# Kernel tuning notes

Measured on AMD Instinct MI355X. Metric: run time of the kernel, lower is better.

The kernel has to match this reference:

```python
import jax, jax.numpy as jnp
import numpy as np

B = 32; H = 56; W = 56; C = 384; NH = 12; WS = 14; SS = 7
L = H * W; N = WS * WS; HD = C // NH; SCALE = HD ** -0.5; HID = 4 * C
NW = (H // WS) * (W // WS)
EPS = 1e-5

def _relative_index():
    ch = np.arange(WS)[:, None].repeat(WS, 1)
    cw = np.arange(WS)[None, :].repeat(WS, 0)
    coords = np.stack([ch, cw], -1).reshape(-1, 2)  # [N,2]
    rel = coords[:, None, :] - coords[None, :, :]
    rel = rel + (WS - 1)
    rel[:, :, 0] *= 2 * WS - 1
    return rel.sum(-1)  # [N,N], values in [0,(2WS-1)^2)

def _attn_mask():
    img = np.zeros((H, W))
    sl = (slice(0, -WS), slice(-WS, -SS), slice(-SS, None))
    cnt = 0
    for hs in sl:
        for ws_ in sl:
            img[hs, ws_] = cnt; cnt += 1
    mw = img.reshape(H // WS, WS, W // WS, WS).transpose(0, 2, 1, 3).reshape(-1, N)
    am = mw[:, None, :] - mw[:, :, None]  # [nW,N,N]
    return np.where(am != 0, -100.0, 0.0).astype(np.float32)

REL_IDX = jnp.asarray(_relative_index())
MASK = jnp.asarray(_attn_mask())  # [NW,N,N]

def _ln(x, w, b):
    m = jnp.mean(x, -1, keepdims=True)
    v = jnp.mean((x - m) ** 2, -1, keepdims=True)
    return (x - m) * jax.lax.rsqrt(v + EPS) * w + b

def setup_inputs() -> dict:
    key = jax.random.key(0)
    ks = jax.random.split(key, 8)
    s = 0.02
    return {
        "x": jax.random.normal(ks[0], (B, L, C), jnp.float32),
        "norm1_w": jnp.ones((C,), jnp.float32),
        "norm1_b": jnp.zeros((C,), jnp.float32),
        "qkv_w": jax.random.normal(ks[1], (3 * C, C), jnp.float32) * s,
        "qkv_b": jnp.zeros((3 * C,), jnp.float32),
        "proj_w": jax.random.normal(ks[2], (C, C), jnp.float32) * s,
        "proj_b": jnp.zeros((C,), jnp.float32),
        "relative_table": jax.random.normal(ks[3], ((2 * WS - 1) ** 2, 2 * NH), jnp.float32) * s,
        "norm2_w": jnp.ones((C,), jnp.float32),
        "norm2_b": jnp.zeros((C,), jnp.float32),
        "fc1_w": jax.random.normal(ks[4], (HID, C), jnp.float32) * s,
        "fc1_b": jnp.zeros((HID,), jnp.float32),
        "fc2_w": jax.random.normal(ks[5], (C, HID), jnp.float32) * s,
        "fc2_b": jnp.zeros((C,), jnp.float32),
    }

def reference(x, norm1_w, norm1_b, qkv_w, qkv_b, proj_w, proj_b,
              relative_table, norm2_w, norm2_b, fc1_w, fc1_b, fc2_w, fc2_b):
    shortcut = x
    xn = _ln(x, norm1_w, norm1_b).reshape(B, H, W, C)
    # cyclic shift + window partition -> [B*NW, N, C]
    xs = jnp.roll(xn, (-SS, -SS), (1, 2))
    xw = xs.reshape(B, H // WS, WS, W // WS, WS, C).transpose(0, 1, 3, 2, 4, 5).reshape(-1, N, C)
    B_ = B * NW
    qkv = (xw @ qkv_w.T + qkv_b).reshape(B_, N, 3, NH, HD).transpose(2, 0, 3, 1, 4)
    q, k, v = qkv[0] * SCALE, qkv[1], qkv[2]  # [B_,NH,N,HD]
    attn = jnp.einsum('bhnd,bhmd->bhnm', q, k)  # [B_,NH,N,N]
    rel = relative_table[REL_IDX]  # [N,N,2*NH]
    rel = rel.transpose(2, 0, 1)  # [2*NH,N,N]
    bias, rscale = rel[:NH], rel[NH:]
    attn = attn + bias[None]
    attn = attn.reshape(B, NW, NH, N, N) + MASK[None, :, None]
    attn = jax.nn.softmax(attn.reshape(B_, NH, N, N), axis=-1)
    attn = attn * rscale[None]  # multiplicative relative scale AFTER softmax
    out = jnp.einsum('bhnm,bhmd->bhnd', attn, v)
    out = out.transpose(0, 2, 1, 3).reshape(B_, N, C)
    out = out @ proj_w.T + proj_b
    # window reverse + reverse shift
    xr = out.reshape(B, H // WS, W // WS, WS, WS, C).transpose(0, 1, 3, 2, 4, 5).reshape(B, H, W, C)
    xr = jnp.roll(xr, (SS, SS), (1, 2)).reshape(B, L, C)
    x = shortcut + xr
    h = _ln(x, norm2_w, norm2_b)
    h = jax.nn.gelu(h @ fc1_w.T + fc1_b, approximate=False) @ fc2_w.T + fc2_b
    return x + h
```

## Files before the change

kernel.cpp:

```cpp
#include <hip/hip_runtime.h>
#include <hip/hip_bf16.h>
#include <math.h>

#define BDIM 32
#define HDIM 56
#define WDIM 56
#define CDIM 384
#define NHEAD 12
#define WSZ 14
#define SSZ 7
#define LDIM (HDIM*WDIM)
#define NTOK (WSZ*WSZ)
#define HDHEAD (CDIM/NHEAD)
#define HIDDIM (4*CDIM)
#define NWIN 16
#define BWIN (BDIM*NWIN)
#define MROWS (BDIM*LDIM)
#define EPSLN 1e-5f
#define ATTSCALE 0.17677669529663687f

typedef __hip_bfloat16 bf16;
typedef __attribute__((ext_vector_type(8))) short bf16x8;
typedef __attribute__((ext_vector_type(4))) float f32x4;

#define ASYNC16(gp, lp) __builtin_amdgcn_global_load_lds( \
    (__attribute__((address_space(1))) void*)(gp),        \
    (__attribute__((address_space(3))) void*)(lp), 16, 0, 0)

static __device__ __forceinline__ short f2bfs(float x) {
  union { bf16 h; short s; } u; u.h = __float2bfloat16(x); return u.s;
}

__global__ __launch_bounds__(256) void k_cvt(const float* __restrict__ in,
                                             bf16* __restrict__ out, int n)
{
  int i = blockIdx.x * 256 + threadIdx.x;
  if (i < n) out[i] = __float2bfloat16(in[i]);
}

template<bool WIN>
__global__ __launch_bounds__(128) void k_ln(const float* __restrict__ xin,
    const float* __restrict__ gw, const float* __restrict__ gb,
    bf16* __restrict__ out)
{
  int r = blockIdx.x;
  int t = threadIdx.x;
  const float* xp = xin + (size_t)r * CDIM;
  float v0 = xp[t], v1 = xp[t+128], v2 = xp[t+256];
  float s  = v0+v1+v2;
  float ss = v0*v0 + v1*v1 + v2*v2;
  #pragma unroll
  for (int o = 32; o > 0; o >>= 1) { s += __shfl_down(s, o); ss += __shfl_down(ss, o); }
  __shared__ float red[4];
  if ((t & 63) == 0) { red[(t>>6)*2] = s; red[(t>>6)*2+1] = ss; }
  __syncthreads();
  float mean = (red[0]+red[2]) * (1.0f/CDIM);
  float var  = (red[1]+red[3]) * (1.0f/CDIM) - mean*mean;
  float rstd = rsqrtf(var + EPSLN);

  size_t orow;
  if (WIN) {
    int b = r / LDIM, l = r % LDIM;
    int h = l / WDIM, w = l % WDIM;
    int h2 = (h + HDIM - SSZ) % HDIM, w2 = (w + WDIM - SSZ) % WDIM;
    int wh = h2 / WSZ, ii = h2 % WSZ, ww = w2 / WSZ, jj = w2 % WSZ;
    int b_ = b*NWIN + wh*4 + ww;
    int n  = ii*WSZ + jj;
    orow = ((size_t)b_*NTOK + n) * CDIM;
  } else {
    orow = (size_t)r * CDIM;
  }
  out[orow+t]     = __float2bfloat16((v0-mean)*rstd*gw[t]     + gb[t]);
  out[orow+t+128] = __float2bfloat16((v1-mean)*rstd*gw[t+128] + gb[t+128]);
  out[orow+t+256] = __float2bfloat16((v2-mean)*rstd*gw[t+256] + gb[t+256]);
}

template<int KD, int EPI>
__global__ __launch_bounds__(256) void k_mgemm(
    const bf16* __restrict__ A, const bf16* __restrict__ Wb,
    const float* __restrict__ bias, const float* __restrict__ aux,
    float* __restrict__ outf, bf16* __restrict__ outb)
{
  __shared__ short As[128*32];
  __shared__ short Bs[128*32];
  int tid  = threadIdx.x;
  int lane = tid & 63, wid = tid >> 6;
  int wr = wid >> 1, wc = wid & 1;
  int row0 = blockIdx.y * 128, col0 = blockIdx.x * 128;

  f32x4 acc[4][4] = {};

  int srow[2];
  int skk = (lane & 3) * 8;
  #pragma unroll
  for (int s = 0; s < 2; s++) {
    int c = wid*2 + s;
    srow[s] = c*16 + (lane >> 2);
  }

  for (int k0 = 0; k0 < KD; k0 += 32) {
    #pragma unroll
    for (int s = 0; s < 2; s++) {
      int c = wid*2 + s;
      ASYNC16(A  + (size_t)(row0 + srow[s])*KD + k0 + skk, &As[c*512]);
      ASYNC16(Wb + (size_t)(col0 + srow[s])*KD + k0 + skk, &Bs[c*512]);
    }
    __syncthreads();

    bf16x8 af[4], bfr[4];
    #pragma unroll
    for (int m = 0; m < 4; m++)
      af[m] = *reinterpret_cast<const bf16x8*>(
          &As[(wr*64 + m*16 + (lane & 15))*32 + ((lane >> 4) * 8)]);
    #pragma unroll
    for (int n = 0; n < 4; n++)
      bfr[n] = *reinterpret_cast<const bf16x8*>(
          &Bs[(wc*64 + n*16 + (lane & 15))*32 + ((lane >> 4) * 8)]);
    #pragma unroll
    for (int m = 0; m < 4; m++)
      #pragma unroll
      for (int n = 0; n < 4; n++)
        acc[m][n] = __builtin_amdgcn_mfma_f32_16x16x32_bf16(af[m], bfr[n], acc[m][n], 0, 0, 0);
    __syncthreads();
  }

  int crow = row0 + wr*64 + ((lane >> 4) * 4);
  int ccol = col0 + wc*64 + (lane & 15);
  #pragma unroll
  for (int m = 0; m < 4; m++) {
    #pragma unroll
    for (int i = 0; i < 4; i++) {
      int r = crow + m*16 + i;
      if constexpr (EPI == 0) {
        int b_ = r / NTOK, nn = r % NTOK;
        const size_t QKVSTRIDE = (size_t)BWIN*NHEAD*NTOK*HDHEAD;
        #pragma unroll
        for (int n = 0; n < 4; n++) {
          int c = ccol + n*16;
          float val = acc[m][n][i] + bias[c];
          int which = c / CDIM, rem = c - which*CDIM;
          int hh = rem >> 5, dd = rem & 31;
          if (which == 0) val *= ATTSCALE;
          outb[(size_t)which*QKVSTRIDE + (((size_t)b_*NHEAD+hh)*NTOK+nn)*HDHEAD + dd]
              = __float2bfloat16(val);
        }
      } else if constexpr (EPI == 1) {
        int b_ = r / NTOK, nn = r % NTOK;
        int b = b_ >> 4, wi = b_ & 15, wh = wi >> 2, ww = wi & 3;
        int ii = nn / WSZ, jj = nn % WSZ;
        int hh = (wh*WSZ + ii + SSZ) % HDIM;
        int wcc = (ww*WSZ + jj + SSZ) % WDIM;
        size_t rr = ((size_t)b*LDIM + hh*WDIM + wcc) * CDIM;
        #pragma unroll
        for (int n = 0; n < 4; n++) {
          int c = ccol + n*16;
          outf[rr+c] = aux[rr+c] + acc[m][n][i] + bias[c];
        }
      } else if constexpr (EPI == 2) {
        #pragma unroll
        for (int n = 0; n < 4; n++) {
          int c = ccol + n*16;
          float val = acc[m][n][i] + bias[c];
          val = 0.5f * val * (1.0f + erff(val * 0.70710678118654752f));
          outb[(size_t)r*HIDDIM + c] = __float2bfloat16(val);
        }
      } else {
        #pragma unroll
        for (int n = 0; n < 4; n++) {
          int c = ccol + n*16;
          outf[(size_t)r*CDIM + c] = acc[m][n][i] + bias[c] + aux[(size_t)r*CDIM + c];
        }
      }
    }
  }
}

__global__ __launch_bounds__(256) void k_attn_mfma(const bf16* __restrict__ q,
    const bf16* __restrict__ k, const bf16* __restrict__ v,
    const float* __restrict__ rt, bf16* __restrict__ out)
{
  __shared__ short  Ks[208*32];
  __shared__ short  Vt[32*224];
  __shared__ short  Ps[4][16*224];
  __shared__ float2 tab2[729];
  __shared__ int    regv[208];

  int blk = blockIdx.x;
  int b_ = blk / NHEAD, head = blk % NHEAD;
  int tid = threadIdx.x, lane = tid & 63, wid = tid >> 6;
  int c15 = lane & 15, h4 = lane >> 4;

  const bf16* kp = k + (size_t)blk*NTOK*HDHEAD;
  const bf16* vp = v + (size_t)blk*NTOK*HDHEAD;
  for (int c = tid; c < 784; c += 256) {
    int m = c >> 2, k8 = (c & 3) * 8;
    *(bf16x8*)&Ks[m*32 + k8] = *(const bf16x8*)(kp + m*32 + k8);
    bf16x8 vv = *(const bf16x8*)(vp + m*32 + k8);
    #pragma unroll
    for (int j = 0; j < 8; j++) Vt[(k8+j)*224 + m] = vv[j];
  }
  for (int e = tid; e < 12*32; e += 256) Ks[196*32 + e] = 0;
  for (int e = tid; e < 32*28; e += 256) Vt[(e/28)*224 + 196 + (e%28)] = 0;
  for (int e = tid; e < 729; e += 256)
    tab2[e] = make_float2(rt[e*2*NHEAD + head], rt[e*2*NHEAD + NHEAD + head]);
  {
    int wi = b_ & 15, wh = wi >> 2, ww = wi & 3;
    for (int e = tid; e < 208; e += 256) {
      int rv = 0;
      if (e < NTOK) {
        int i = e / WSZ, j = e % WSZ;
        int ha = wh*WSZ + i, wa = ww*WSZ + j;
        int rh = ha < (HDIM-WSZ) ? 0 : (ha < (HDIM-SSZ) ? 1 : 2);
        int rw = wa < (WDIM-WSZ) ? 0 : (wa < (WDIM-SSZ) ? 1 : 2);
        rv = rh*3 + rw;
      }
      regv[e] = rv;
    }
  }
  __syncthreads();

  int   moff[13], mreg[13];
  float mpad[13];
  #pragma unroll
  for (int t = 0; t < 13; t++) {
    int m  = t*16 + c15;
    int mm = min(m, NTOK-1);
    moff[t] = (mm/WSZ)*27 + (mm%WSZ);
    mreg[t] = regv[mm];
    mpad[t] = (m >= NTOK) ? -1e30f : 0.f;
  }

  short* myP = &Ps[wid][0];
  #pragma unroll
  for (int i = 0; i < 4; i++) myP[(h4*4+i)*224 + 208 + c15] = 0;

  bf16* op = out + (size_t)b_*NTOK*CDIM + head*HDHEAD;

  for (int t4 = 0; t4 < 4; t4++) {
    int s = t4*4 + wid;
    int qrow = min(s*16 + c15, NTOK-1);
    bf16x8 qf = *(const bf16x8*)(q + ((size_t)blk*NTOK + qrow)*HDHEAD + h4*8);

    f32x4 sc[13];
    #pragma unroll
    for (int t = 0; t < 13; t++) {
      bf16x8 kf = *(const bf16x8*)&Ks[(t*16 + c15)*32 + h4*8];
      sc[t] = __builtin_amdgcn_mfma_f32_16x16x32_bf16(qf, kf, (f32x4){0.f,0.f,0.f,0.f}, 0, 0, 0);
    }

    #pragma unroll
    for (int i = 0; i < 4; i++) {
      int n  = s*16 + h4*4 + i;
      int nc = min(n, NTOK-1);
      int nbase = ((nc/WSZ) + 13)*27 + (nc%WSZ) + 13;
      int nreg  = regv[nc];
      float rr[13];
      float mx = -1e30f;
      #pragma unroll
      for (int t = 0; t < 13; t++) {
        float2 hr = tab2[nbase - moff[t]];
        float sv = sc[t][i] + hr.x + ((mreg[t] != nreg) ? -100.f : 0.f) + mpad[t];
        rr[t] = hr.y;
        sc[t][i] = sv;
        mx = fmaxf(mx, sv);
      }
      #pragma unroll
      for (int o = 1; o < 16; o <<= 1) mx = fmaxf(mx, __shfl_xor(mx, o));
      float sum = 0.f;
      #pragma unroll
      for (int t = 0; t < 13; t++) {
        float e = __expf(sc[t][i] - mx);
        sc[t][i] = e; sum += e;
      }
      #pragma unroll
      for (int o = 1; o < 16; o <<= 1) sum += __shfl_xor(sum, o);
      float inv = 1.f / sum;
      int prow = h4*4 + i;
      #pragma unroll
      for (int t = 0; t < 13; t++)
        myP[prow*224 + t*16 + c15] = f2bfs(sc[t][i] * inv * rr[t]);
    }

    __syncthreads();

    f32x4 o0 = {0.f,0.f,0.f,0.f}, o1 = {0.f,0.f,0.f,0.f};
    #pragma unroll
    for (int t7 = 0; t7 < 7; t7++) {
      bf16x8 pf = *(const bf16x8*)&myP[c15*224 + t7*32 + h4*8];
      bf16x8 v0 = *(const bf16x8*)&Vt[c15*224 + t7*32 + h4*8];
      bf16x8 v1 = *(const bf16x8*)&Vt[(16 + c15)*224 + t7*32 + h4*8];
      o0 = __builtin_amdgcn_mfma_f32_16x16x32_bf16(pf, v0, o0, 0, 0, 0);
      o1 = __builtin_amdgcn_mfma_f32_16x16x32_bf16(pf, v1, o1, 0, 0, 0);
    }

    #pragma unroll
    for (int i = 0; i < 4; i++) {
      int n = s*16 + h4*4 + i;
      if (n < NTOK) {
        op[(size_t)n*CDIM + c15]      = __float2bfloat16(o0[i]);
        op[(size_t)n*CDIM + 16 + c15] = __float2bfloat16(o1[i]);
      }
    }

    __syncthreads();
  }
}

extern "C" void kernel_launch(void* const* d_in, const int* in_sizes, int n_in,
                              void* d_out, int out_size, void* d_ws, size_t ws_size,
                              hipStream_t stream)
{
  const float* x      = (const float*)d_in[0];
  const float* n1w    = (const float*)d_in[1];
  const float* n1b    = (const float*)d_in[2];
  const float* qkv_w  = (const float*)d_in[3];
  const float* qkv_b  = (const float*)d_in[4];
  const float* proj_w = (const float*)d_in[5];
  const float* proj_b = (const float*)d_in[6];
  const float* rt     = (const float*)d_in[7];
  const float* n2w    = (const float*)d_in[8];
  const float* n2b    = (const float*)d_in[9];
  const float* fc1_w  = (const float*)d_in[10];
  const float* fc1_b  = (const float*)d_in[11];
  const float* fc2_w  = (const float*)d_in[12];
  const float* fc2_b  = (const float*)d_in[13];

  char* ws = (char*)d_ws;
  const size_t SZ_BF = (size_t)MROWS * CDIM * 2;
  bf16*  xw      = (bf16*)ws;
  bf16*  attnout = (bf16*)ws;
  bf16*  qkv     = (bf16*)(ws + SZ_BF);
  float* x2      = (float*)(ws + SZ_BF);
  bf16*  hln     = (bf16*)(ws + 3*SZ_BF);
  bf16*  hid     = (bf16*)(ws + 4*SZ_BF);
  const int NQKVW = 3*CDIM*CDIM;
  const int NPROJW = CDIM*CDIM;
  const int NFCW  = HIDDIM*CDIM;
  bf16* wq  = (bf16*)(ws + 4*SZ_BF);
  bf16* wp  = wq + NQKVW;
  bf16* wf1 = (bf16*)ws;
  bf16* wf2 = wf1 + NFCW;
  const size_t QKVSTRIDE = (size_t)BWIN*NHEAD*NTOK*HDHEAD;

  k_cvt<<<(NQKVW+255)/256, 256, 0, stream>>>(qkv_w, wq, NQKVW);
  k_cvt<<<(NPROJW+255)/256, 256, 0, stream>>>(proj_w, wp, NPROJW);

  k_ln<true><<<MROWS, 128, 0, stream>>>(x, n1w, n1b, xw);
  k_mgemm<CDIM, 0><<<dim3((3*CDIM)/128, MROWS/128), 256, 0, stream>>>(
      xw, wq, qkv_b, nullptr, nullptr, qkv);
  k_attn_mfma<<<BWIN*NHEAD, 256, 0, stream>>>(
      qkv, qkv + QKVSTRIDE, qkv + 2*QKVSTRIDE, rt, attnout);
  k_mgemm<CDIM, 1><<<dim3(CDIM/128, MROWS/128), 256, 0, stream>>>(
      attnout, wp, proj_b, x, x2, nullptr);

  k_cvt<<<(NFCW+255)/256, 256, 0, stream>>>(fc1_w, wf1, NFCW);
  k_cvt<<<(NFCW+255)/256, 256, 0, stream>>>(fc2_w, wf2, NFCW);

  k_ln<false><<<MROWS, 128, 0, stream>>>(x2, n2w, n2b, hln);
  k_mgemm<CDIM, 2><<<dim3(HIDDIM/128, MROWS/128), 256, 0, stream>>>(
      hln, wf1, fc1_b, nullptr, nullptr, hid);
  k_mgemm<HIDDIM, 3><<<dim3(CDIM/128, MROWS/128), 256, 0, stream>>>(
      hid, wf2, fc2_b, x2, (float*)d_out, nullptr);
}
```

Before: 1.194 ms.

## Store residual stream in bf16 and pad attention LDS rows to avoid bank conflicts

The intermediate residual x2 (shortcut plus projection) is now stored as bf16 instead of fp32. LayerNorm2 and the fc2 residual epilogue read it as bf16, which halves the memory traffic for that tensor. Separately, the attention kernel's K, V-transposed and P shared-memory tiles get padded row strides (40/232) to reduce LDS bank conflicts. Rounding the residual to bf16 before adding the MLP output loses precision in the final result.

```diff
diff --git a/kernel.cpp b/kernel.cpp
--- a/kernel.cpp
+++ b/kernel.cpp
@@ -19,6 +19,10 @@
 #define EPSLN 1e-5f
 #define ATTSCALE 0.17677669529663687f
 
+#define KROW 40
+#define VROW 232
+#define PROW 232
+
 typedef __hip_bfloat16 bf16;
 typedef __attribute__((ext_vector_type(8))) short bf16x8;
 typedef __attribute__((ext_vector_type(4))) float f32x4;
@@ -30,6 +34,8 @@
 static __device__ __forceinline__ short f2bfs(float x) {
   union { bf16 h; short s; } u; u.h = __float2bfloat16(x); return u.s;
 }
+static __device__ __forceinline__ float tof(float x) { return x; }
+static __device__ __forceinline__ float tof(bf16 x)  { return __bfloat162float(x); }
 
 __global__ __launch_bounds__(256) void k_cvt(const float* __restrict__ in,
                                              bf16* __restrict__ out, int n)
@@ -38,15 +44,15 @@
   if (i < n) out[i] = __float2bfloat16(in[i]);
 }
 
-template<bool WIN>
-__global__ __launch_bounds__(128) void k_ln(const float* __restrict__ xin,
+template<bool WIN, typename TIN>
+__global__ __launch_bounds__(128) void k_ln(const TIN* __restrict__ xin,
     const float* __restrict__ gw, const float* __restrict__ gb,
     bf16* __restrict__ out)
 {
   int r = blockIdx.x;
   int t = threadIdx.x;
-  const float* xp = xin + (size_t)r * CDIM;
-  float v0 = xp[t], v1 = xp[t+128], v2 = xp[t+256];
+  const TIN* xp = xin + (size_t)r * CDIM;
+  float v0 = tof(xp[t]), v1 = tof(xp[t+128]), v2 = tof(xp[t+256]);
   float s  = v0+v1+v2;
   float ss = v0*v0 + v1*v1 + v2*v2;
   #pragma unroll
@@ -79,6 +85,7 @@
 __global__ __launch_bounds__(256) void k_mgemm(
     const bf16* __restrict__ A, const bf16* __restrict__ Wb,
     const float* __restrict__ bias, const float* __restrict__ aux,
+    const bf16* __restrict__ auxb,
     float* __restrict__ outf, bf16* __restrict__ outb)
 {
   __shared__ short As[128*32];
@@ -154,7 +161,7 @@
         #pragma unroll
         for (int n = 0; n < 4; n++) {
           int c = ccol + n*16;
-          outf[rr+c] = aux[rr+c] + acc[m][n][i] + bias[c];
+          outb[rr+c] = __float2bfloat16(aux[rr+c] + acc[m][n][i] + bias[c]);
         }
       } else if constexpr (EPI == 2) {
         #pragma unroll
@@ -168,7 +175,8 @@
         #pragma unroll
         for (int n = 0; n < 4; n++) {
           int c = ccol + n*16;
-          outf[(size_t)r*CDIM + c] = acc[m][n][i] + bias[c] + aux[(size_t)r*CDIM + c];
+          outf[(size_t)r*CDIM + c] = acc[m][n][i] + bias[c]
+              + __bfloat162float(auxb[(size_t)r*CDIM + c]);
         }
       }
     }
@@ -179,9 +187,9 @@
     const bf16* __restrict__ k, const bf16* __restrict__ v,
     const float* __restrict__ rt, bf16* __restrict__ out)
 {
-  __shared__ short  Ks[208*32];
-  __shared__ short  Vt[32*224];
-  __shared__ short  Ps[4][16*224];
+  __shared__ short  Ks[208*KROW];
+  __shared__ short  Vt[32*VROW];
+  __shared__ short  Ps[4][16*PROW];
   __shared__ float2 tab2[729];
   __shared__ int    regv[208];
 
@@ -194,13 +202,13 @@
   const bf16* vp = v + (size_t)blk*NTOK*HDHEAD;
   for (int c = tid; c < 784; c += 256) {
     int m = c >> 2, k8 = (c & 3) * 8;
-    *(bf16x8*)&Ks[m*32 + k8] = *(const bf16x8*)(kp + m*32 + k8);
+    *(bf16x8*)&Ks[m*KROW + k8] = *(const bf16x8*)(kp + m*32 + k8);
     bf16x8 vv = *(const bf16x8*)(vp + m*32 + k8);
     #pragma unroll
-    for (int j = 0; j < 8; j++) Vt[(k8+j)*224 + m] = vv[j];
-  }
-  for (int e = tid; e < 12*32; e += 256) Ks[196*32 + e] = 0;
-  for (int e = tid; e < 32*28; e += 256) Vt[(e/28)*224 + 196 + (e%28)] = 0;
+    for (int j = 0; j < 8; j++) Vt[(k8+j)*VROW + m] = vv[j];
+  }
+  for (int e = tid; e < 12*KROW; e += 256) Ks[196*KROW + e] = 0;
+  for (int e = tid; e < 32*28; e += 256) Vt[(e/28)*VROW + 196 + (e%28)] = 0;
   for (int e = tid; e < 729; e += 256)
     tab2[e] = make_float2(rt[e*2*NHEAD + head], rt[e*2*NHEAD + NHEAD + head]);
   {
@@ -232,7 +240,7 @@
 
   short* myP = &Ps[wid][0];
   #pragma unroll
-  for (int i = 0; i < 4; i++) myP[(h4*4+i)*224 + 208 + c15] = 0;
+  for (int i = 0; i < 4; i++) myP[(h4*4+i)*PROW + 208 + c15] = 0;
 
   bf16* op = out + (size_t)b_*NTOK*CDIM + head*HDHEAD;
 
@@ -244,7 +252,7 @@
     f32x4 sc[13];
     #pragma unroll
     for (int t = 0; t < 13; t++) {
-      bf16x8 kf = *(const bf16x8*)&Ks[(t*16 + c15)*32 + h4*8];
+      bf16x8 kf = *(const bf16x8*)&Ks[(t*16 + c15)*KROW + h4*8];
       sc[t] = __builtin_amdgcn_mfma_f32_16x16x32_bf16(qf, kf, (f32x4){0.f,0.f,0.f,0.f}, 0, 0, 0);
     }
 
@@ -278,7 +286,7 @@
       int prow = h4*4 + i;
       #pragma unroll
       for (int t = 0; t < 13; t++)
-        myP[prow*224 + t*16 + c15] = f2bfs(sc[t][i] * inv * rr[t]);
+        myP[prow*PROW + t*16 + c15] = f2bfs(sc[t][i] * inv * rr[t]);
     }
 
     __syncthreads();
@@ -286,9 +294,9 @@
     f32x4 o0 = {0.f,0.f,0.f,0.f}, o1 = {0.f,0.f,0.f,0.f};
     #pragma unroll
     for (int t7 = 0; t7 < 7; t7++) {
-      bf16x8 pf = *(const bf16x8*)&myP[c15*224 + t7*32 + h4*8];
-      bf16x8 v0 = *(const bf16x8*)&Vt[c15*224 + t7*32 + h4*8];
-      bf16x8 v1 = *(const bf16x8*)&Vt[(16 + c15)*224 + t7*32 + h4*8];
+      bf16x8 pf = *(const bf16x8*)&myP[c15*PROW + t7*32 + h4*8];
+      bf16x8 v0 = *(const bf16x8*)&Vt[c15*VROW + t7*32 + h4*8];
+      bf16x8 v1 = *(const bf16x8*)&Vt[(16 + c15)*VROW + t7*32 + h4*8];
       o0 = __builtin_amdgcn_mfma_f32_16x16x32_bf16(pf, v0, o0, 0, 0, 0);
       o1 = __builtin_amdgcn_mfma_f32_16x16x32_bf16(pf, v1, o1, 0, 0, 0);
     }
@@ -330,8 +338,8 @@
   bf16*  xw      = (bf16*)ws;
   bf16*  attnout = (bf16*)ws;
   bf16*  qkv     = (bf16*)(ws + SZ_BF);
-  float* x2      = (float*)(ws + SZ_BF);
-  bf16*  hln     = (bf16*)(ws + 3*SZ_BF);
+  bf16*  x2b     = (bf16*)(ws + SZ_BF);
+  bf16*  hln     = (bf16*)(ws + 2*SZ_BF);
   bf16*  hid     = (bf16*)(ws + 4*SZ_BF);
   const int NQKVW = 3*CDIM*CDIM;
   const int NPROJW = CDIM*CDIM;
@@ -345,20 +353,20 @@
   k_cvt<<<(NQKVW+255)/256, 256, 0, stream>>>(qkv_w, wq, NQKVW);
   k_cvt<<<(NPROJW+255)/256, 256, 0, stream>>>(proj_w, wp, NPROJW);
 
-  k_ln<true><<<MROWS, 128, 0, stream>>>(x, n1w, n1b, xw);
+  k_ln<true, float><<<MROWS, 128, 0, stream>>>(x, n1w, n1b, xw);
   k_mgemm<CDIM, 0><<<dim3((3*CDIM)/128, MROWS/128), 256, 0, stream>>>(
-      xw, wq, qkv_b, nullptr, nullptr, qkv);
+      xw, wq, qkv_b, nullptr, nullptr, nullptr, qkv);
   k_attn_mfma<<<BWIN*NHEAD, 256, 0, stream>>>(
       qkv, qkv + QKVSTRIDE, qkv + 2*QKVSTRIDE, rt, attnout);
   k_mgemm<CDIM, 1><<<dim3(CDIM/128, MROWS/128), 256, 0, stream>>>(
-      attnout, wp, proj_b, x, x2, nullptr);
+      attnout, wp, proj_b, x, nullptr, nullptr, x2b);
 
   k_cvt<<<(NFCW+255)/256, 256, 0, stream>>>(fc1_w, wf1, NFCW);
   k_cvt<<<(NFCW+255)/256, 256, 0, stream>>>(fc2_w, wf2, NFCW);
 
-  k_ln<false><<<MROWS, 128, 0, stream>>>(x2, n2w, n2b, hln);
+  k_ln<false, bf16><<<MROWS, 128, 0, stream>>>(x2b, n2w, n2b, hln);
   k_mgemm<CDIM, 2><<<dim3(HIDDIM/128, MROWS/128), 256, 0, stream>>>(
-      hln, wf1, fc1_b, nullptr, nullptr, hid);
+      hln, wf1, fc1_b, nullptr, nullptr, nullptr, hid);
   k_mgemm<HIDDIM, 3><<<dim3(CDIM/128, MROWS/128), 256, 0, stream>>>(
-      hid, wf2, fc2_b, x2, (float*)d_out, nullptr);
-}
+      hid, wf2, fc2_b, nullptr, x2b, (float*)d_out, nullptr);
+}
```

New measurement: 1.154 ms. 1.04x faster.
